# Kernel optimization log

Measured on AMD Instinct MI355X. Metric: run time of the kernel, lower is better.

The kernel has to match this reference:

```python
import jax, jax.numpy as jnp
import numpy as np

N_OBJ, N_REG = 4096, 8192
D_HO = D_HR = 512
GATE_W = 128
E = 131072


def setup_inputs() -> dict:
    key = jax.random.key(0)
    ks = jax.random.split(key, 10)
    s = 1.0 / np.sqrt(D_HO + D_HR)
    return {
        "feature_obj": jax.random.normal(ks[0], (N_OBJ, D_HO), jnp.float32),
        "feature_region": jax.random.normal(ks[1], (N_REG, D_HR), jnp.float32),
        # edge lists (tgt, src) equivalent to np.where(select_mat > 0)
        "r2o_tgt": jnp.sort(jax.random.randint(ks[2], (E,), 0, N_OBJ, jnp.int32)),
        "r2o_src": jax.random.randint(ks[3], (E,), 0, N_REG, jnp.int32),
        "o2r_tgt": jnp.sort(jax.random.randint(ks[4], (E,), 0, N_REG, jnp.int32)),
        "o2r_src": jax.random.randint(ks[5], (E,), 0, N_OBJ, jnp.int32),
        # attention gate Linear(dim_src+dim_tgt -> gate_width), bias=True
        "gw_r2o": jax.random.uniform(ks[6], (GATE_W, D_HR + D_HO), jnp.float32, -s, s),
        "gb_r2o": jnp.zeros((GATE_W,), jnp.float32),
        "gw_o2r": jax.random.uniform(ks[7], (GATE_W, D_HO + D_HR), jnp.float32, -s, s),
        "gb_o2r": jnp.zeros((GATE_W,), jnp.float32),
        # transform Sequential(ReLU, Linear(dim -> dim, bias=True))
        "tw_r2o": jax.random.uniform(ks[8], (D_HO, D_HR), jnp.float32, -s, s),
        "tb_r2o": jnp.zeros((D_HO,), jnp.float32),
        "tw_o2r": jax.random.uniform(ks[9], (D_HR, D_HO), jnp.float32, -s, s),
        "tb_o2r": jnp.zeros((D_HR,), jnp.float32),
    }


def _message(tgt_feat, src_feat, tgt_idx, src_idx, gw, gb, num_tgt):
    # gather per-edge source/target features: [E, ds], [E, dt]
    src = src_feat[src_idx]
    tgt = tgt_feat[tgt_idx]
    # Attention_Module: gate = mean(sigmoid(W @ relu(cat(src, tgt)) + b))
    g = jax.nn.relu(jnp.concatenate([src, tgt], axis=-1))
    gate = jnp.mean(jax.nn.sigmoid(g @ gw.T + gb), axis=-1, keepdims=True)  # [E, 1]
    msg = src * gate
    agg = jax.ops.segment_sum(msg, tgt_idx, num_segments=num_tgt)
    # mps_use_average=True -> per-target mean; targets with no edges stay zero
    cnt = jax.ops.segment_sum(jnp.ones((tgt_idx.shape[0], 1), msg.dtype), tgt_idx, num_segments=num_tgt)
    return agg / jnp.maximum(cnt, 1.0)


def reference(feature_obj, feature_region, r2o_tgt, r2o_src, o2r_tgt, o2r_src,
              gw_r2o, gb_r2o, gw_o2r, gb_o2r, tw_r2o, tb_r2o, tw_o2r, tb_o2r):
    m_r2o = _message(feature_obj, feature_region, r2o_tgt, r2o_src, gw_r2o, gb_r2o, N_OBJ)
    out_obj = feature_obj + jax.nn.relu(m_r2o) @ tw_r2o.T + tb_r2o
    m_o2r = _message(feature_region, feature_obj, o2r_tgt, o2r_src, gw_o2r, gb_o2r, N_REG)
    out_reg = feature_region + jax.nn.relu(m_o2r) @ tw_o2r.T + tb_o2r
    return (out_obj, out_reg)
```

## Files before the change

kernel.cpp:

```cpp
#include <hip/hip_runtime.h>

constexpr int N_OBJ = 4096, N_REG = 8192, D = 512, GW = 128, NE = 131072;

typedef __attribute__((ext_vector_type(8))) short short8;
typedef __attribute__((ext_vector_type(4))) float f32x4;

__device__ inline short f2bf(float f) {
  unsigned u = __builtin_bit_cast(unsigned, f);
  unsigned r = (u + 0x7FFF + ((u >> 16) & 1)) >> 16;
  return (short)r;
}
__device__ inline float bf2f(short s) {
  return __builtin_bit_cast(float, (unsigned)(((unsigned short)s) << 16));
}

__global__ __launch_bounds__(256) void cast_csr(
    const float* __restrict__ feat_reg, const float* __restrict__ feat_obj,
    const float* __restrict__ gw_r2o, const float* __restrict__ gw_o2r,
    const float* __restrict__ tw_r2o, const float* __restrict__ tw_o2r,
    const int* __restrict__ t_r2o, const int* __restrict__ t_o2r,
    short* __restrict__ raw_reg, short* __restrict__ relu_reg,
    short* __restrict__ raw_obj, short* __restrict__ relu_obj,
    short* __restrict__ Wreg, short* __restrict__ Wobj,
    short* __restrict__ btw_r2o, short* __restrict__ btw_o2r,
    int* __restrict__ off_r2o, int* __restrict__ off_o2r) {
  int i = blockIdx.x * 256 + threadIdx.x;
  if (i >= 1769472) {
    i -= 1769472;
    const int* tgt; int* off; int t;
    if (i <= N_OBJ) { tgt = t_r2o; off = off_r2o; t = i; }
    else {
      i -= N_OBJ + 1;
      if (i > N_REG) return;
      tgt = t_o2r; off = off_o2r; t = i;
    }
    int lo = 0, hi = NE;
    while (lo < hi) {
      int mid = (lo + hi) >> 1;
      if (tgt[mid] < t) lo = mid + 1; else hi = mid;
    }
    off[t] = lo;
    return;
  }
  if (i < 1572864) {
    const float* src; short* draw; short* drelu; int j = i;
    if (j < 1048576) { src = feat_reg; draw = raw_reg; drelu = relu_reg; }
    else { j -= 1048576; src = feat_obj; draw = raw_obj; drelu = relu_obj; }
    float4 v = ((const float4*)src)[j];
    ((short4*)draw)[j] = make_short4(f2bf(v.x), f2bf(v.y), f2bf(v.z), f2bf(v.w));
    ((short4*)drelu)[j] = make_short4(f2bf(fmaxf(v.x, 0.f)), f2bf(fmaxf(v.y, 0.f)),
                                      f2bf(fmaxf(v.z, 0.f)), f2bf(fmaxf(v.w, 0.f)));
    return;
  }
  i -= 1572864;
  const float* src; short* dst; int di;
  if (i < 32768) {
    int row = i >> 7, c4 = i & 127;
    src = (row < 128) ? gw_r2o + (size_t)row * 1024 + c4 * 4
                      : gw_o2r + (size_t)(row - 128) * 1024 + 512 + c4 * 4;
    dst = Wreg; di = i;
  } else if (i < 65536) {
    int k = i - 32768, row = k >> 7, c4 = k & 127;
    src = (row < 128) ? gw_r2o + (size_t)row * 1024 + 512 + c4 * 4
                      : gw_o2r + (size_t)(row - 128) * 1024 + c4 * 4;
    dst = Wobj; di = k;
  } else if (i < 131072) { di = i - 65536; src = tw_r2o + (size_t)di * 4; dst = btw_r2o; }
  else                   { di = i - 131072; src = tw_o2r + (size_t)di * 4; dst = btw_o2r; }
  float4 v = *(const float4*)src;
  ((short4*)dst)[di] = make_short4(f2bf(v.x), f2bf(v.y), f2bf(v.z), f2bf(v.w));
}

struct GemmPair {
  const short* A[2]; const short* B[2];
  const float* res[2]; const float* bias[2];
  void* C[2];
  int nb0;
  int nxb;
  int ldc;
};

template<bool EPI>
__global__ __launch_bounds__(256) void gemm_pair(GemmPair gp) {
  __shared__ short As[128 * 32];
  __shared__ short Bs[128 * 32];
  int b = blockIdx.x;
  const int pi = (b >= gp.nb0) ? 1 : 0;
  if (pi) b -= gp.nb0;
  const int bx = b % gp.nxb, by = b / gp.nxb;
  const short* __restrict__ A = gp.A[pi];
  const short* __restrict__ B = gp.B[pi];
  const int ldc = gp.ldc;
  const int tid = threadIdx.x;
  const int lane = tid & 63, w = tid >> 6;
  const int m0 = by * 128, n0 = bx * 128;
  const int wm = (w >> 1) * 64, wn = (w & 1) * 64;
  const int sr = lane >> 2, sc = (lane & 3) * 8;
  const int fr = lane & 15, fk = (lane >> 4) * 8;

  f32x4 acc[4][4];
#pragma unroll
  for (int i = 0; i < 4; ++i)
#pragma unroll
    for (int j = 0; j < 4; ++j) acc[i][j] = (f32x4){0.f, 0.f, 0.f, 0.f};

  for (int k0 = 0; k0 < 512; k0 += 32) {
#pragma unroll
    for (int h = 0; h < 2; ++h) {
      int rg = w * 32 + h * 16;
      const short* ga = A + (size_t)(m0 + rg + sr) * 512 + k0 + sc;
      const short* gb = B + (size_t)(n0 + rg + sr) * 512 + k0 + sc;
      __builtin_amdgcn_global_load_lds(
          (const __attribute__((address_space(1))) void*)ga,
          (__attribute__((address_space(3))) void*)&As[rg * 32], 16, 0, 0);
      __builtin_amdgcn_global_load_lds(
          (const __attribute__((address_space(1))) void*)gb,
          (__attribute__((address_space(3))) void*)&Bs[rg * 32], 16, 0, 0);
    }
    __syncthreads();
    short8 a[4], bfr[4];
#pragma unroll
    for (int i = 0; i < 4; ++i)
      a[i] = *(const short8*)&As[(wm + i * 16 + fr) * 32 + fk];
#pragma unroll
    for (int j = 0; j < 4; ++j)
      bfr[j] = *(const short8*)&Bs[(wn + j * 16 + fr) * 32 + fk];
#pragma unroll
    for (int i = 0; i < 4; ++i)
#pragma unroll
      for (int j = 0; j < 4; ++j)
        acc[i][j] = __builtin_amdgcn_mfma_f32_16x16x32_bf16(a[i], bfr[j], acc[i][j], 0, 0, 0);
    __syncthreads();
  }

  if (EPI) {
    float* C = (float*)gp.C[pi];
    const float* res = gp.res[pi];
    const float* bias = gp.bias[pi];
#pragma unroll
    for (int i = 0; i < 4; ++i)
#pragma unroll
      for (int j = 0; j < 4; ++j) {
        int n = n0 + wn + j * 16 + fr;
#pragma unroll
        for (int r = 0; r < 4; ++r) {
          int m = m0 + wm + i * 16 + (lane >> 4) * 4 + r;
          C[(size_t)m * ldc + n] = acc[i][j][r] + res[(size_t)m * ldc + n] + bias[n];
        }
      }
  } else {
    short* C = (short*)gp.C[pi];
#pragma unroll
    for (int i = 0; i < 4; ++i)
#pragma unroll
      for (int j = 0; j < 4; ++j) {
        int n = n0 + wn + j * 16 + fr;
#pragma unroll
        for (int r = 0; r < 4; ++r) {
          int m = m0 + wm + i * 16 + (lane >> 4) * 4 + r;
          C[(size_t)m * ldc + n] = f2bf(acc[i][j][r]);
        }
      }
  }
}

__global__ __launch_bounds__(256) void fused_msg(
    const short* __restrict__ Preg, const short* __restrict__ Pobj,
    const short* __restrict__ raw_reg, const short* __restrict__ raw_obj,
    const int* __restrict__ r2o_src, const int* __restrict__ o2r_src,
    const int* __restrict__ off_r2o, const int* __restrict__ off_o2r,
    const float* __restrict__ gb_r2o, const float* __restrict__ gb_o2r,
    short* __restrict__ m_obj, short* __restrict__ m_reg) {
  __shared__ float red[4][512];
  int t = blockIdx.x;
  const short* PA; const short* PB; const short* feat; const int* src;
  const int* off; const float* gb; short* mo; int po;
  if (t < N_OBJ) {
    PA = Preg; PB = Pobj; feat = raw_reg; src = r2o_src; off = off_r2o;
    gb = gb_r2o; mo = m_obj; po = 0;
  } else {
    t -= N_OBJ;
    PA = Pobj; PB = Preg; feat = raw_obj; src = o2r_src; off = off_o2r;
    gb = gb_o2r; mo = m_reg; po = 128;
  }
  const int tid = threadIdx.x, lane = tid & 63, w = tid >> 6;
  const int e0 = off[t], e1 = off[t + 1];
  short2 pb2 = *(const short2*)&PB[(size_t)t * 256 + po + lane * 2];
  float2 gb2 = *(const float2*)&gb[lane * 2];
  const float c0 = bf2f(pb2.x) + gb2.x, c1 = bf2f(pb2.y) + gb2.y;
  float acc[8] = {};
  for (int e = e0 + w; e < e1; e += 4) {
    int s = src[e];
    short2 pa2 = *(const short2*)&PA[(size_t)s * 256 + po + lane * 2];
    short8 v = *(const short8*)&feat[(size_t)s * 512 + lane * 8];
    float gs = 1.f / (1.f + __expf(-(bf2f(pa2.x) + c0)))
             + 1.f / (1.f + __expf(-(bf2f(pa2.y) + c1)));
#pragma unroll
    for (int msk = 32; msk >= 1; msk >>= 1) gs += __shfl_xor(gs, msk, 64);
    gs *= (1.0f / 128.0f);
#pragma unroll
    for (int j = 0; j < 8; ++j) acc[j] += bf2f(v[j]) * gs;
  }
  *(float4*)&red[w][lane * 8]     = (float4){acc[0], acc[1], acc[2], acc[3]};
  *(float4*)&red[w][lane * 8 + 4] = (float4){acc[4], acc[5], acc[6], acc[7]};
  __syncthreads();
  const float inv = 1.0f / fmaxf((float)(e1 - e0), 1.0f);
  const int d = tid * 2;
  float s0 = red[0][d] + red[1][d] + red[2][d] + red[3][d];
  float s1 = red[0][d + 1] + red[1][d + 1] + red[2][d + 1] + red[3][d + 1];
  short2 o;
  o.x = f2bf(fmaxf(s0 * inv, 0.f));
  o.y = f2bf(fmaxf(s1 * inv, 0.f));
  *(short2*)(mo + (size_t)t * 512 + d) = o;
}

extern "C" void kernel_launch(void* const* d_in, const int* in_sizes, int n_in,
                              void* d_out, int out_size, void* d_ws, size_t ws_size,
                              hipStream_t stream) {
  const float* feat_obj = (const float*)d_in[0];
  const float* feat_reg = (const float*)d_in[1];
  const int*   r2o_tgt  = (const int*)d_in[2];
  const int*   r2o_src  = (const int*)d_in[3];
  const int*   o2r_tgt  = (const int*)d_in[4];
  const int*   o2r_src  = (const int*)d_in[5];
  const float* gw_r2o   = (const float*)d_in[6];
  const float* gb_r2o   = (const float*)d_in[7];
  const float* gw_o2r   = (const float*)d_in[8];
  const float* gb_o2r   = (const float*)d_in[9];
  const float* tw_r2o   = (const float*)d_in[10];
  const float* tb_r2o   = (const float*)d_in[11];
  const float* tw_o2r   = (const float*)d_in[12];
  const float* tb_o2r   = (const float*)d_in[13];
  float* out_obj = (float*)d_out;
  float* out_reg = out_obj + (size_t)N_OBJ * D;

  size_t cur = 0;
  auto alloc = [&](size_t bytes) -> void* {
    cur = (cur + 255) & ~(size_t)255;
    void* p = (char*)d_ws + cur;
    cur += bytes;
    return p;
  };
  int*   off_r2o = (int*)alloc((N_OBJ + 1) * sizeof(int));
  int*   off_o2r = (int*)alloc((N_REG + 1) * sizeof(int));
  short* raw_reg = (short*)alloc((size_t)N_REG * D * 2);
  short* relu_reg= (short*)alloc((size_t)N_REG * D * 2);
  short* raw_obj = (short*)alloc((size_t)N_OBJ * D * 2);
  short* relu_obj= (short*)alloc((size_t)N_OBJ * D * 2);
  short* Wreg    = (short*)alloc((size_t)256 * D * 2);
  short* Wobj    = (short*)alloc((size_t)256 * D * 2);
  short* btw_r2o = (short*)alloc((size_t)D * D * 2);
  short* btw_o2r = (short*)alloc((size_t)D * D * 2);
  short* Preg    = (short*)alloc((size_t)N_REG * 256 * 2);
  short* Pobj    = (short*)alloc((size_t)N_OBJ * 256 * 2);
  short* m_obj   = (short*)alloc((size_t)N_OBJ * D * 2);
  short* m_reg   = (short*)alloc((size_t)N_REG * D * 2);

  cast_csr<<<6961, 256, 0, stream>>>(feat_reg, feat_obj, gw_r2o, gw_o2r, tw_r2o, tw_o2r,
                                     r2o_tgt, o2r_tgt,
                                     raw_reg, relu_reg, raw_obj, relu_obj,
                                     Wreg, Wobj, btw_r2o, btw_o2r, off_r2o, off_o2r);

  GemmPair proj;
  proj.A[0] = relu_reg; proj.B[0] = Wreg; proj.C[0] = Preg;
  proj.A[1] = relu_obj; proj.B[1] = Wobj; proj.C[1] = Pobj;
  proj.res[0] = proj.res[1] = nullptr; proj.bias[0] = proj.bias[1] = nullptr;
  proj.nb0 = 2 * (N_REG / 128); proj.nxb = 2; proj.ldc = 256;
  gemm_pair<false><<<192, 256, 0, stream>>>(proj);

  fused_msg<<<N_OBJ + N_REG, 256, 0, stream>>>(Preg, Pobj, raw_reg, raw_obj,
                                               r2o_src, o2r_src, off_r2o, off_o2r,
                                               gb_r2o, gb_o2r, m_obj, m_reg);

  GemmPair tr;
  tr.A[0] = m_reg; tr.B[0] = btw_o2r; tr.res[0] = feat_reg; tr.bias[0] = tb_o2r; tr.C[0] = out_reg;
  tr.A[1] = m_obj; tr.B[1] = btw_r2o; tr.res[1] = feat_obj; tr.bias[1] = tb_r2o; tr.C[1] = out_obj;
  tr.nb0 = 4 * (N_REG / 128); tr.nxb = 4; tr.ldc = D;
  gemm_pair<true><<<384, 256, 0, stream>>>(tr);
}
```

Measured before the change: 197.7 us.

## Store gathered features and gate projections in FP8 and widen per-lane edge work

Raw source features and the gate projection outputs are now stored as FP8 (e4m3 via packed convert) instead of bf16. This halves the bytes gathered per edge in the message kernel, which is dominated by random row gathers. The message loop is also restructured so that each half-wave handles its own edge: lanes take 16 features and 4 gate columns, and the gate mean scale is folded into the final normalization. The cost is a larger loss of precision in the message features and gate logits, which may threaten tolerance, and the GEMM epilogue now writes single bytes.

Result: faster. 186.0 us (-6.0%).

```diff
diff --git a/kernel.cpp b/kernel.cpp
--- a/kernel.cpp
+++ b/kernel.cpp
@@ -4,6 +4,7 @@
 
 typedef __attribute__((ext_vector_type(8))) short short8;
 typedef __attribute__((ext_vector_type(4))) float f32x4;
+typedef __attribute__((ext_vector_type(2))) float f32x2;
 
 __device__ inline short f2bf(float f) {
   unsigned u = __builtin_bit_cast(unsigned, f);
@@ -19,8 +20,8 @@
     const float* __restrict__ gw_r2o, const float* __restrict__ gw_o2r,
     const float* __restrict__ tw_r2o, const float* __restrict__ tw_o2r,
     const int* __restrict__ t_r2o, const int* __restrict__ t_o2r,
-    short* __restrict__ raw_reg, short* __restrict__ relu_reg,
-    short* __restrict__ raw_obj, short* __restrict__ relu_obj,
+    unsigned char* __restrict__ raw_reg, short* __restrict__ relu_reg,
+    unsigned char* __restrict__ raw_obj, short* __restrict__ relu_obj,
     short* __restrict__ Wreg, short* __restrict__ Wobj,
     short* __restrict__ btw_r2o, short* __restrict__ btw_o2r,
     int* __restrict__ off_r2o, int* __restrict__ off_o2r) {
@@ -43,11 +44,13 @@
     return;
   }
   if (i < 1572864) {
-    const float* src; short* draw; short* drelu; int j = i;
+    const float* src; unsigned char* draw; short* drelu; int j = i;
     if (j < 1048576) { src = feat_reg; draw = raw_reg; drelu = relu_reg; }
     else { j -= 1048576; src = feat_obj; draw = raw_obj; drelu = relu_obj; }
     float4 v = ((const float4*)src)[j];
-    ((short4*)draw)[j] = make_short4(f2bf(v.x), f2bf(v.y), f2bf(v.z), f2bf(v.w));
+    int p = __builtin_amdgcn_cvt_pk_fp8_f32(v.x, v.y, 0, false);
+    p = __builtin_amdgcn_cvt_pk_fp8_f32(v.z, v.w, p, true);
+    ((unsigned*)draw)[j] = (unsigned)p;
     ((short4*)drelu)[j] = make_short4(f2bf(fmaxf(v.x, 0.f)), f2bf(fmaxf(v.y, 0.f)),
                                       f2bf(fmaxf(v.z, 0.f)), f2bf(fmaxf(v.w, 0.f)));
     return;
@@ -148,7 +151,7 @@
         }
       }
   } else {
-    short* C = (short*)gp.C[pi];
+    unsigned char* C = (unsigned char*)gp.C[pi];
 #pragma unroll
     for (int i = 0; i < 4; ++i)
 #pragma unroll
@@ -157,23 +160,24 @@
 #pragma unroll
         for (int r = 0; r < 4; ++r) {
           int m = m0 + wm + i * 16 + (lane >> 4) * 4 + r;
-          C[(size_t)m * ldc + n] = f2bf(acc[i][j][r]);
+          int pk = __builtin_amdgcn_cvt_pk_fp8_f32(acc[i][j][r], acc[i][j][r], 0, false);
+          C[(size_t)m * ldc + n] = (unsigned char)(pk & 0xFF);
         }
       }
   }
 }
 
 __global__ __launch_bounds__(256) void fused_msg(
-    const short* __restrict__ Preg, const short* __restrict__ Pobj,
-    const short* __restrict__ raw_reg, const short* __restrict__ raw_obj,
+    const unsigned char* __restrict__ Preg, const unsigned char* __restrict__ Pobj,
+    const unsigned char* __restrict__ raw_reg, const unsigned char* __restrict__ raw_obj,
     const int* __restrict__ r2o_src, const int* __restrict__ o2r_src,
     const int* __restrict__ off_r2o, const int* __restrict__ off_o2r,
     const float* __restrict__ gb_r2o, const float* __restrict__ gb_o2r,
     short* __restrict__ m_obj, short* __restrict__ m_reg) {
   __shared__ float red[4][512];
   int t = blockIdx.x;
-  const short* PA; const short* PB; const short* feat; const int* src;
-  const int* off; const float* gb; short* mo; int po;
+  const unsigned char *PA, *PB, *feat; const int *src, *off; const float* gb;
+  short* mo; int po;
   if (t < N_OBJ) {
     PA = Preg; PB = Pobj; feat = raw_reg; src = r2o_src; off = off_r2o;
     gb = gb_r2o; mo = m_obj; po = 0;
@@ -183,27 +187,54 @@
     gb = gb_o2r; mo = m_reg; po = 128;
   }
   const int tid = threadIdx.x, lane = tid & 63, w = tid >> 6;
+  const int hw = lane >> 5, l = lane & 31;
   const int e0 = off[t], e1 = off[t + 1];
-  short2 pb2 = *(const short2*)&PB[(size_t)t * 256 + po + lane * 2];
-  float2 gb2 = *(const float2*)&gb[lane * 2];
-  const float c0 = bf2f(pb2.x) + gb2.x, c1 = bf2f(pb2.y) + gb2.y;
-  float acc[8] = {};
-  for (int e = e0 + w; e < e1; e += 4) {
+  unsigned pbu = *(const unsigned*)&PB[(size_t)t * 256 + po + l * 4];
+  f32x2 pb01 = __builtin_amdgcn_cvt_pk_f32_fp8((int)pbu, false);
+  f32x2 pb23 = __builtin_amdgcn_cvt_pk_f32_fp8((int)pbu, true);
+  float4 gbv = *(const float4*)&gb[l * 4];
+  const float c0 = pb01.x + gbv.x, c1 = pb01.y + gbv.y;
+  const float c2 = pb23.x + gbv.z, c3 = pb23.y + gbv.w;
+  float acc[16] = {};
+  for (int e = e0 + w * 2 + hw; e < e1; e += 8) {
     int s = src[e];
-    short2 pa2 = *(const short2*)&PA[(size_t)s * 256 + po + lane * 2];
-    short8 v = *(const short8*)&feat[(size_t)s * 512 + lane * 8];
-    float gs = 1.f / (1.f + __expf(-(bf2f(pa2.x) + c0)))
-             + 1.f / (1.f + __expf(-(bf2f(pa2.y) + c1)));
-#pragma unroll
-    for (int msk = 32; msk >= 1; msk >>= 1) gs += __shfl_xor(gs, msk, 64);
-    gs *= (1.0f / 128.0f);
-#pragma unroll
-    for (int j = 0; j < 8; ++j) acc[j] += bf2f(v[j]) * gs;
-  }
-  *(float4*)&red[w][lane * 8]     = (float4){acc[0], acc[1], acc[2], acc[3]};
-  *(float4*)&red[w][lane * 8 + 4] = (float4){acc[4], acc[5], acc[6], acc[7]};
+    unsigned pau = *(const unsigned*)&PA[(size_t)s * 256 + po + l * 4];
+    uint4 fv = *(const uint4*)&feat[(size_t)s * 512 + l * 16];
+    f32x2 a01 = __builtin_amdgcn_cvt_pk_f32_fp8((int)pau, false);
+    f32x2 a23 = __builtin_amdgcn_cvt_pk_f32_fp8((int)pau, true);
+    float gs = 1.f / (1.f + __expf(-(a01.x + c0)))
+             + 1.f / (1.f + __expf(-(a01.y + c1)))
+             + 1.f / (1.f + __expf(-(a23.x + c2)))
+             + 1.f / (1.f + __expf(-(a23.y + c3)));
+#pragma unroll
+    for (int msk = 16; msk >= 1; msk >>= 1) gs += __shfl_xor(gs, msk, 64);
+    f32x2 f0 = __builtin_amdgcn_cvt_pk_f32_fp8((int)fv.x, false);
+    f32x2 f1 = __builtin_amdgcn_cvt_pk_f32_fp8((int)fv.x, true);
+    f32x2 f2 = __builtin_amdgcn_cvt_pk_f32_fp8((int)fv.y, false);
+    f32x2 f3 = __builtin_amdgcn_cvt_pk_f32_fp8((int)fv.y, true);
+    f32x2 f4 = __builtin_amdgcn_cvt_pk_f32_fp8((int)fv.z, false);
+    f32x2 f5 = __builtin_amdgcn_cvt_pk_f32_fp8((int)fv.z, true);
+    f32x2 f6 = __builtin_amdgcn_cvt_pk_f32_fp8((int)fv.w, false);
+    f32x2 f7 = __builtin_amdgcn_cvt_pk_f32_fp8((int)fv.w, true);
+    acc[0]  += f0.x * gs; acc[1]  += f0.y * gs;
+    acc[2]  += f1.x * gs; acc[3]  += f1.y * gs;
+    acc[4]  += f2.x * gs; acc[5]  += f2.y * gs;
+    acc[6]  += f3.x * gs; acc[7]  += f3.y * gs;
+    acc[8]  += f4.x * gs; acc[9]  += f4.y * gs;
+    acc[10] += f5.x * gs; acc[11] += f5.y * gs;
+    acc[12] += f6.x * gs; acc[13] += f6.y * gs;
+    acc[14] += f7.x * gs; acc[15] += f7.y * gs;
+  }
+#pragma unroll
+  for (int jj = 0; jj < 16; ++jj) acc[jj] += __shfl_xor(acc[jj], 32, 64);
+  if (hw == 0) {
+#pragma unroll
+    for (int q = 0; q < 4; ++q)
+      *(float4*)&red[w][l * 16 + q * 4] =
+          (float4){acc[q * 4], acc[q * 4 + 1], acc[q * 4 + 2], acc[q * 4 + 3]};
+  }
   __syncthreads();
-  const float inv = 1.0f / fmaxf((float)(e1 - e0), 1.0f);
+  const float inv = (1.0f / 128.0f) / fmaxf((float)(e1 - e0), 1.0f);
   const int d = tid * 2;
   float s0 = red[0][d] + red[1][d] + red[2][d] + red[3][d];
   float s1 = red[0][d + 1] + red[1][d + 1] + red[2][d + 1] + red[3][d + 1];
@@ -242,16 +273,16 @@
   };
   int*   off_r2o = (int*)alloc((N_OBJ + 1) * sizeof(int));
   int*   off_o2r = (int*)alloc((N_REG + 1) * sizeof(int));
-  short* raw_reg = (short*)alloc((size_t)N_REG * D * 2);
+  unsigned char* raw_reg = (unsigned char*)alloc((size_t)N_REG * D);
+  unsigned char* raw_obj = (unsigned char*)alloc((size_t)N_OBJ * D);
   short* relu_reg= (short*)alloc((size_t)N_REG * D * 2);
-  short* raw_obj = (short*)alloc((size_t)N_OBJ * D * 2);
   short* relu_obj= (short*)alloc((size_t)N_OBJ * D * 2);
   short* Wreg    = (short*)alloc((size_t)256 * D * 2);
   short* Wobj    = (short*)alloc((size_t)256 * D * 2);
   short* btw_r2o = (short*)alloc((size_t)D * D * 2);
   short* btw_o2r = (short*)alloc((size_t)D * D * 2);
-  short* Preg    = (short*)alloc((size_t)N_REG * 256 * 2);
-  short* Pobj    = (short*)alloc((size_t)N_OBJ * 256 * 2);
+  unsigned char* Preg = (unsigned char*)alloc((size_t)N_REG * 256);
+  unsigned char* Pobj = (unsigned char*)alloc((size_t)N_OBJ * 256);
   short* m_obj   = (short*)alloc((size_t)N_OBJ * D * 2);
   short* m_reg   = (short*)alloc((size_t)N_REG * D * 2);
 
```
